# Kernel optimization log

Measured on AMD Instinct MI355X. Metric: run time of the kernel, lower is better.

Reference implementation:

```python
import jax, jax.numpy as jnp
import numpy as np

V, T, C, H, L = 32000, 1024, 768, 12, 6
HS = C // H
B = 4
EPS = 1e-5


def layernorm(x, g, b):
    mu = jnp.mean(x, axis=-1, keepdims=True)
    var = jnp.mean(jnp.square(x - mu), axis=-1, keepdims=True)
    return (x - mu) * jax.lax.rsqrt(var + EPS) * g + b


def setup_inputs() -> dict:
    key = jax.random.key(0)
    ks = iter(jax.random.split(key, 24))
    s = lambda *sh: jax.random.normal(next(ks), sh, dtype=jnp.float32) * 0.02
    inp = {
        "tokens": jax.random.randint(next(ks), (B, T), 0, V, dtype=jnp.int64),
        "tok_emb": s(V, C),
        "pos_emb": s(T, C),
        "ln1_g": jnp.ones((L, C), jnp.float32), "ln1_b": jnp.zeros((L, C), jnp.float32),
        "wq": s(L, C, C), "wk": s(L, C, C), "wv": s(L, C, C),
        "wo": s(L, C, C), "bo": jnp.zeros((L, C), jnp.float32),
        "ln2_g": jnp.ones((L, C), jnp.float32), "ln2_b": jnp.zeros((L, C), jnp.float32),
        "w1": s(L, C, 4 * C), "b1": jnp.zeros((L, 4 * C), jnp.float32),
        "w2": s(L, 4 * C, C), "b2": jnp.zeros((L, C), jnp.float32),
        "lnf_g": jnp.ones((C,), jnp.float32), "lnf_b": jnp.zeros((C,), jnp.float32),
        "lm_w": s(C, V), "lm_b": jnp.zeros((V,), jnp.float32),
    }
    return inp


def reference(tokens, tok_emb, pos_emb, ln1_g, ln1_b, wq, wk, wv, wo, bo,
              ln2_g, ln2_b, w1, b1, w2, b2, lnf_g, lnf_b, lm_w, lm_b):
    x = tok_emb[tokens] + pos_emb[:T]  # [B,T,C]
    causal = jnp.tril(jnp.ones((T, T), bool))
    scale = HS ** -0.5
    for l in range(L):
        h = layernorm(x, ln1_g[l], ln1_b[l])
        q = (h @ wq[l]).reshape(B, T, H, HS)
        k = (h @ wk[l]).reshape(B, T, H, HS)
        v = (h @ wv[l]).reshape(B, T, H, HS)
        att = jnp.einsum("bthd,bshd->bhts", q, k) * scale
        att = jnp.where(causal, att, -jnp.inf)
        wei = jax.nn.softmax(att, axis=-1)
        o = jnp.einsum("bhts,bshd->bthd", wei, v).reshape(B, T, C)
        x = o @ wo[l] + bo[l] + x
        h2 = layernorm(x, ln2_g[l], ln2_b[l])
        x = jax.nn.relu(h2 @ w1[l] + b1[l]) @ w2[l] + b2[l] + x
    x = layernorm(x, lnf_g, lnf_b)
    logits = x @ lm_w + lm_b  # [B,T,V]
    return logits
```

## Files before the change

kernel.cpp:

```cpp
#include <hip/hip_runtime.h>

static constexpr int kV = 32000, kT = 1024, kC = 768, kH = 12, kL = 6, kB = 4;
static constexpr int kF = 3072;
static constexpr int kM = kB * kT;
static constexpr float kNEG = -30000.f;

typedef __attribute__((ext_vector_type(8))) __bf16 bf16x8;
typedef __attribute__((ext_vector_type(4))) float  f32x4;

#define DEV __device__ __forceinline__

DEV void gload16(const void* g, void* l) {
  __builtin_amdgcn_global_load_lds((__attribute__((address_space(1))) void*)(g),
                                   (__attribute__((address_space(3))) void*)(l), 16, 0, 0);
}

__global__ __launch_bounds__(192) void embed_k(const int* __restrict__ tokens,
                                               const float* __restrict__ tok_emb,
                                               const float* __restrict__ pos_emb,
                                               float* __restrict__ x) {
  int row = blockIdx.x, tid = threadIdx.x;
  int tok = tokens[row];
  int t   = row & (kT - 1);
  const float4* te = (const float4*)(tok_emb + (size_t)tok * kC);
  const float4* pe = (const float4*)(pos_emb + (size_t)t * kC);
  float4 a = te[tid], p = pe[tid];
  float4 r; r.x = a.x + p.x; r.y = a.y + p.y; r.z = a.z + p.z; r.w = a.w + p.w;
  ((float4*)(x + (size_t)row * kC))[tid] = r;
}

__global__ __launch_bounds__(256) void ln_k(const float* __restrict__ x,
                                            const float* __restrict__ g,
                                            const float* __restrict__ b,
                                            __bf16* __restrict__ out) {
  int row = blockIdx.x, tid = threadIdx.x;
  const float* xr = x + (size_t)row * kC;
  float v0 = xr[tid], v1 = xr[tid + 256], v2 = xr[tid + 512];
  float s = v0 + v1 + v2;
#pragma unroll
  for (int m = 1; m < 64; m <<= 1) s += __shfl_xor(s, m, 64);
  __shared__ float red1[4], red2[4];
  int wid = tid >> 6;
  if ((tid & 63) == 0) red1[wid] = s;
  __syncthreads();
  float mu = (red1[0] + red1[1] + red1[2] + red1[3]) * (1.f / kC);
  float d0 = v0 - mu, d1 = v1 - mu, d2 = v2 - mu;
  float q = d0 * d0 + d1 * d1 + d2 * d2;
#pragma unroll
  for (int m = 1; m < 64; m <<= 1) q += __shfl_xor(q, m, 64);
  if ((tid & 63) == 0) red2[wid] = q;
  __syncthreads();
  float var = (red2[0] + red2[1] + red2[2] + red2[3]) * (1.f / kC);
  float rs = rsqrtf(var + 1e-5f);
  __bf16* o = out + (size_t)row * kC;
  o[tid]       = (__bf16)(d0 * rs * g[tid]       + b[tid]);
  o[tid + 256] = (__bf16)(d1 * rs * g[tid + 256] + b[tid + 256]);
  o[tid + 512] = (__bf16)(d2 * rs * g[tid + 512] + b[tid + 512]);
}

__global__ __launch_bounds__(256) void convT_k(const float* __restrict__ in,
                                               __bf16* __restrict__ out,
                                               int R, int Cc, size_t in_ls, size_t out_ls) {
  __shared__ float tile[32][33];
  const float* inp  = in  + (size_t)blockIdx.z * in_ls;
  __bf16*      outp = out + (size_t)blockIdx.z * out_ls;
  int r0 = blockIdx.y * 32, c0 = blockIdx.x * 32;
  int tx = threadIdx.x & 31, ty = threadIdx.x >> 5;
#pragma unroll
  for (int i = 0; i < 32; i += 8)
    tile[ty + i][tx] = inp[(size_t)(r0 + ty + i) * Cc + c0 + tx];
  __syncthreads();
#pragma unroll
  for (int i = 0; i < 32; i += 8)
    outp[(size_t)(c0 + ty + i) * R + r0 + tx] = (__bf16)tile[tx][ty + i];
}

DEV void tile_decode(int gx, int gy, int& mt, int& nt) {
  int nwg  = gx * gy;
  int wgid = blockIdx.y * gx + blockIdx.x;
  int q8 = nwg >> 3;
  int xcd = wgid & 7, loc = wgid >> 3;
  int sid = xcd * q8 + loc;
  int band = gx << 3;
  int c = sid / band, rem = sid % band;
  nt = rem >> 3;
  mt = (c << 3) + (rem & 7);
}

__global__ __launch_bounds__(512, 1) void gemmHD_k(const __bf16* __restrict__ A,
                                                   const __bf16* __restrict__ Bt,
                                                   const float* __restrict__ bias,
                                                   float* __restrict__ Cout,
                                                   int M, int N, int K) {
  __shared__ char lds[131072];
  int tid = threadIdx.x, lane = tid & 63, wid = tid >> 6;
  int wm = wid >> 2, wn = wid & 3;
  int mt, ntile;
  tile_decode(gridDim.x, gridDim.y, mt, ntile);
  int m0 = mt * 256, n0 = ntile * 256;
  int fr = lane & 15, fg = lane >> 4;
  f32x4 acc[8][4] = {};
  const size_t ldab = (size_t)K * 2;
  int nt = K >> 6;

  auto STAGE = [&](char* base, int t) {
    int k0 = t << 6;
#pragma unroll
    for (int it = 0; it < 4; ++it) {
      int oo  = tid * 16 + it * 8192;
      int row = oo >> 7;
      int cb  = (oo & 127) ^ ((row & 7) << 4);
      gload16((const char*)A + (size_t)(m0 + row) * ldab + (size_t)k0 * 2 + cb,
              base + it * 8192 + wid * 1024);
    }
#pragma unroll
    for (int it = 0; it < 4; ++it) {
      int oo  = tid * 16 + it * 8192;
      int row = oo >> 7;
      int cb  = (oo & 127) ^ ((row & 7) << 4);
      gload16((const char*)Bt + (size_t)(n0 + row) * ldab + (size_t)k0 * 2 + cb,
              base + 32768 + it * 8192 + wid * 1024);
    }
  };

  STAGE(lds, 0);
  asm volatile("s_waitcnt vmcnt(0)" ::: "memory");
  __builtin_amdgcn_sched_barrier(0);
  __builtin_amdgcn_s_barrier();

  for (int t = 0; t < nt; ++t) {
    char* base = lds + (t & 1) * 65536;
    const char* Ab = base;
    const char* Bb = base + 32768;
    if (t + 1 < nt) STAGE(lds + ((t + 1) & 1) * 65536, t + 1);

    __builtin_amdgcn_s_setprio(1);
    bf16x8 bfr[4];
#pragma unroll
    for (int p = 0; p < 4; ++p) {
      const int ks = p >> 1, mh = p & 1;
      const int cc = ks * 64 + fg * 16;
      if (mh == 0) {
#pragma unroll
        for (int n = 0; n < 4; ++n) {
          int row = wn * 64 + n * 16 + fr;
          bfr[n] = *(const bf16x8*)(Bb + row * 128 + (cc ^ ((row & 7) << 4)));
        }
      }
      bf16x8 af[4];
#pragma unroll
      for (int i = 0; i < 4; ++i) {
        int row = wm * 128 + mh * 64 + i * 16 + fr;
        af[i] = *(const bf16x8*)(Ab + row * 128 + (cc ^ ((row & 7) << 4)));
      }
#pragma unroll
      for (int i = 0; i < 4; ++i)
#pragma unroll
        for (int n = 0; n < 4; ++n)
          acc[mh * 4 + i][n] = __builtin_amdgcn_mfma_f32_16x16x32_bf16(
              af[i], bfr[n], acc[mh * 4 + i][n], 0, 0, 0);
    }
    __builtin_amdgcn_s_setprio(0);

    __builtin_amdgcn_s_barrier();
    if (t + 1 < nt)
      asm volatile("s_waitcnt vmcnt(0)" ::: "memory");
    __builtin_amdgcn_sched_barrier(0);
    __builtin_amdgcn_s_barrier();
  }

#pragma unroll
  for (int mi = 0; mi < 8; ++mi) {
#pragma unroll
    for (int n = 0; n < 4; ++n) {
      int cg  = n0 + wn * 64 + n * 16 + fr;
      int rgb = m0 + wm * 128 + mi * 16 + fg * 4;
      float bv = bias[cg];
#pragma unroll
      for (int r = 0; r < 4; ++r)
        Cout[(size_t)(rgb + r) * N + cg] = acc[mi][n][r] + bv;
    }
  }
}

template <int EPI>
__global__ __launch_bounds__(256) void gemm128_k(const __bf16* __restrict__ A,
                                                 const __bf16* __restrict__ Bt,
                                                 const float* __restrict__ bias,
                                                 const float* res,
                                                 void* Cout,
                                                 int M, int N, int K) {
  __shared__ char lds[65536];
  int tid = threadIdx.x, lane = tid & 63, wid = tid >> 6;
  int wr = wid >> 1, wc = wid & 1;
  int mt, ntile;
  tile_decode(gridDim.x, gridDim.y, mt, ntile);
  int m0 = mt * 128, n0 = ntile * 128;
  int fr = lane & 15, fg = lane >> 4;
  f32x4 acc[4][4] = {};
  const size_t ldab = (size_t)K * 2;

  auto STAGE = [&](int buf, int t) {
    int k0 = t << 6;
    char* base = lds + buf * 32768;
#pragma unroll
    for (int it = 0; it < 4; ++it) {
      int oo  = tid * 16 + it * 4096;
      int row = oo >> 7;
      int cb  = (oo & 127) ^ ((row & 7) << 4);
      gload16((const char*)A  + (size_t)(m0 + row) * ldab + (size_t)k0 * 2 + cb,
              base + it * 4096 + wid * 1024);
      gload16((const char*)Bt + (size_t)(n0 + row) * ldab + (size_t)k0 * 2 + cb,
              base + 16384 + it * 4096 + wid * 1024);
    }
  };
  auto COMPUTE = [&](int buf) {
    char* base = lds + buf * 32768;
#pragma unroll
    for (int kk = 0; kk < 2; ++kk) {
      int cb = (kk * 64 + (fg << 4)) ^ ((lane & 7) << 4);
      bf16x8 af[4], bfr[4];
#pragma unroll
      for (int i = 0; i < 4; ++i) {
        af[i]  = *(const bf16x8*)(base         + (wr * 64 + i * 16 + fr) * 128 + cb);
        bfr[i] = *(const bf16x8*)(base + 16384 + (wc * 64 + i * 16 + fr) * 128 + cb);
      }
#pragma unroll
      for (int i = 0; i < 4; ++i)
#pragma unroll
        for (int j = 0; j < 4; ++j)
          acc[i][j] = __builtin_amdgcn_mfma_f32_16x16x32_bf16(af[i], bfr[j], acc[i][j], 0, 0, 0);
    }
  };

  int nt = K >> 6;
  STAGE(0, 0);
  STAGE(1, 1);
  asm volatile("s_waitcnt vmcnt(8)" ::: "memory");
  __builtin_amdgcn_sched_barrier(0);
  __builtin_amdgcn_s_barrier();
  int cur = 0;
  for (int t = 0; t < nt; ++t) {
    __builtin_amdgcn_s_setprio(1);
    COMPUTE(cur);
    __builtin_amdgcn_s_setprio(0);
    if (t + 1 < nt) {
      __builtin_amdgcn_s_barrier();
      if (t + 2 < nt) {
        STAGE(cur, t + 2);
        asm volatile("s_waitcnt vmcnt(8)" ::: "memory");
      } else {
        asm volatile("s_waitcnt vmcnt(0)" ::: "memory");
      }
      __builtin_amdgcn_sched_barrier(0);
      __builtin_amdgcn_s_barrier();
      cur ^= 1;
    }
  }

#pragma unroll
  for (int i = 0; i < 4; ++i) {
#pragma unroll
    for (int j = 0; j < 4; ++j) {
      int cg  = n0 + wc * 64 + j * 16 + fr;
      int rgb = m0 + wr * 64 + i * 16 + fg * 4;
      if constexpr (EPI == 4) {
        if (n0 < 1536) {
#pragma unroll
          for (int r = 0; r < 4; ++r)
            ((__bf16*)Cout)[(size_t)(rgb + r) * 1536 + cg] = (__bf16)acc[i][j][r];
        } else {
          int d = cg - 1536;
          ushort4 pk;
          unsigned short* pp = (unsigned short*)&pk;
#pragma unroll
          for (int r = 0; r < 4; ++r) {
            __bf16 bv = (__bf16)acc[i][j][r];
            pp[r] = *(unsigned short*)&bv;
          }
          __bf16* vT = (__bf16*)const_cast<float*>(res);
          *(ushort4*)(vT + (size_t)d * kM + rgb) = pk;
        }
      } else if constexpr (EPI == 1) {
        float bv = bias[cg];
#pragma unroll
        for (int r = 0; r < 4; ++r) {
          float v = acc[i][j][r] + bv;
          ((__bf16*)Cout)[(size_t)(rgb + r) * N + cg] = (__bf16)fmaxf(v, 0.f);
        }
      } else {
        float bv = bias[cg];
#pragma unroll
        for (int r = 0; r < 4; ++r) {
          float v = acc[i][j][r] + bv;
          size_t idx = (size_t)(rgb + r) * N + cg;
          ((float*)Cout)[idx] = v + res[idx];
        }
      }
    }
  }
}

__global__ __launch_bounds__(256) void attn_k(const __bf16* __restrict__ qk,
                                              const __bf16* __restrict__ vT,
                                              __bf16* __restrict__ optr) {
  __shared__ char lds[40960];
  int tid = threadIdx.x, lane = tid & 63, wid = tid >> 6;
  int qt = blockIdx.x, hh = blockIdx.y, bb = blockIdx.z;
  size_t rowbase = (size_t)bb * kT;
  int qr = qt * 64 + wid * 16;
  char* Psw = lds + 32768 + wid * 2048;

  bf16x8 qf[2];
  {
    const __bf16* p = qk + (rowbase + qr + (lane & 15)) * (2 * kC) + hh * 64 + ((lane >> 4) * 8);
    qf[0] = *(const bf16x8*)p;
    qf[1] = *(const bf16x8*)(p + 32);
  }
  f32x4 oacc[4] = {};
  float mrun[4] = {kNEG, kNEG, kNEG, kNEG};
  float lrun[4] = {0.f, 0.f, 0.f, 0.f};

  bf16x8 kr[2], vr[2];
  auto LOADT = [&](int st) {
    int s0 = st * 64;
#pragma unroll
    for (int it = 0; it < 2; ++it) {
      int oo  = tid * 16 + it * 4096;
      int row = oo >> 7;
      int cb  = (oo & 127) ^ ((row & 7) << 4);
      kr[it] = *(const bf16x8*)((const char*)qk +
                 ((rowbase + s0 + row) * (2 * kC) + kC + hh * 64) * 2 + cb);
      vr[it] = *(const bf16x8*)((const char*)vT +
                 ((size_t)(hh * 64 + row) * kM + rowbase + s0) * 2 + cb);
    }
  };
  auto WRITET = [&](int buf) {
    char* b = lds + buf * 16384;
#pragma unroll
    for (int it = 0; it < 2; ++it) {
      int oo = tid * 16 + it * 4096;
      *(bf16x8*)(b + oo)        = kr[it];
      *(bf16x8*)(b + 8192 + oo) = vr[it];
    }
  };

  LOADT(0);
  WRITET(0);
  if (qt >= 1) LOADT(1);

  for (int st = 0; st <= qt; ++st) {
    int cur = st & 1;
    char* kb = lds + cur * 16384;
    char* vb = kb + 8192;
    __syncthreads();
    if (st + 1 <= qt) {
      WRITET(cur ^ 1);
      if (st + 2 <= qt) LOADT(st + 2);
    }

    int s0 = st * 64;
    f32x4 sacc[4] = {};
#pragma unroll
    for (int kk = 0; kk < 2; ++kk) {
      int cb = (kk * 64 + ((lane >> 4) << 4)) ^ ((lane & 7) << 4);
#pragma unroll
      for (int j = 0; j < 4; ++j) {
        bf16x8 kf = *(const bf16x8*)(kb + (j * 16 + (lane & 15)) * 128 + cb);
        sacc[j] = __builtin_amdgcn_mfma_f32_16x16x32_bf16(qf[kk], kf, sacc[j], 0, 0, 0);
      }
    }

    float pv[4][4], vm[4] = {kNEG, kNEG, kNEG, kNEG};
#pragma unroll
    for (int j = 0; j < 4; ++j) {
      int scol = s0 + j * 16 + (lane & 15);
#pragma unroll
      for (int r = 0; r < 4; ++r) {
        int qrow = qr + (lane >> 4) * 4 + r;
        float sv = sacc[j][r] * 0.125f;
        if (scol > qrow) sv = kNEG;
        pv[j][r] = sv;
        vm[r] = fmaxf(vm[r], sv);
      }
    }
#pragma unroll
    for (int r = 0; r < 4; ++r) {
      float v = vm[r];
      v = fmaxf(v, __shfl_xor(v, 1, 64)); v = fmaxf(v, __shfl_xor(v, 2, 64));
      v = fmaxf(v, __shfl_xor(v, 4, 64)); v = fmaxf(v, __shfl_xor(v, 8, 64));
      float mnew = fmaxf(mrun[r], v);
      float sc = __expf(mrun[r] - mnew);
      mrun[r] = mnew;
      lrun[r] *= sc;
      oacc[0][r] *= sc; oacc[1][r] *= sc; oacc[2][r] *= sc; oacc[3][r] *= sc;
      float rsum = 0.f;
#pragma unroll
      for (int j = 0; j < 4; ++j) {
        float p = __expf(pv[j][r] - mnew);
        pv[j][r] = p;
        rsum += p;
      }
      rsum += __shfl_xor(rsum, 1, 64); rsum += __shfl_xor(rsum, 2, 64);
      rsum += __shfl_xor(rsum, 4, 64); rsum += __shfl_xor(rsum, 8, 64);
      lrun[r] += rsum;
    }

#pragma unroll
    for (int j = 0; j < 4; ++j)
#pragma unroll
      for (int r = 0; r < 4; ++r) {
        int rloc = (lane >> 4) * 4 + r;
        int cbyt = (2 * (j * 16 + (lane & 15))) ^ ((rloc & 7) << 4);
        *(__bf16*)(Psw + rloc * 128 + cbyt) = (__bf16)pv[j][r];
      }

#pragma unroll
    for (int kk = 0; kk < 2; ++kk) {
      int cb = (kk * 64 + ((lane >> 4) << 4)) ^ ((lane & 7) << 4);
      bf16x8 pf = *(const bf16x8*)(Psw + (lane & 15) * 128 + cb);
#pragma unroll
      for (int j = 0; j < 4; ++j) {
        bf16x8 vf = *(const bf16x8*)(vb + (j * 16 + (lane & 15)) * 128 + cb);
        oacc[j] = __builtin_amdgcn_mfma_f32_16x16x32_bf16(pf, vf, oacc[j], 0, 0, 0);
      }
    }
  }

#pragma unroll
  for (int r = 0; r < 4; ++r) {
    float inv = lrun[r] > 0.f ? 1.f / lrun[r] : 0.f;
#pragma unroll
    for (int j = 0; j < 4; ++j) {
      int cg = hh * 64 + j * 16 + (lane & 15);
      int rg = qr + (lane >> 4) * 4 + r;
      optr[(rowbase + rg) * kC + cg] = (__bf16)(oacc[j][r] * inv);
    }
  }
}

extern "C" void kernel_launch(void* const* d_in, const int* in_sizes, int n_in,
                              void* d_out, int out_size, void* d_ws, size_t ws_size,
                              hipStream_t stream) {
  (void)in_sizes; (void)n_in; (void)out_size; (void)ws_size;
  const int*   tokens  = (const int*)  d_in[0];
  const float* tok_emb = (const float*)d_in[1];
  const float* pos_emb = (const float*)d_in[2];
  const float* ln1_g   = (const float*)d_in[3];
  const float* ln1_b   = (const float*)d_in[4];
  const float* wq      = (const float*)d_in[5];
  const float* wk      = (const float*)d_in[6];
  const float* wv      = (const float*)d_in[7];
  const float* wo      = (const float*)d_in[8];
  const float* bo      = (const float*)d_in[9];
  const float* ln2_g   = (const float*)d_in[10];
  const float* ln2_b   = (const float*)d_in[11];
  const float* w1      = (const float*)d_in[12];
  const float* b1      = (const float*)d_in[13];
  const float* w2      = (const float*)d_in[14];
  const float* b2      = (const float*)d_in[15];
  const float* lnf_g   = (const float*)d_in[16];
  const float* lnf_b   = (const float*)d_in[17];
  const float* lm_w    = (const float*)d_in[18];
  const float* lm_b    = (const float*)d_in[19];
  float* out = (float*)d_out;

  char* ws = (char*)d_ws;
  size_t off = 0;
  auto alloc = [&](size_t bytes) -> char* {
    char* p = ws + off; off += (bytes + 255) & ~(size_t)255; return p;
  };
  float*  x    = (float*) alloc((size_t)kM * kC * 4);
  __bf16* h    = (__bf16*)alloc((size_t)kM * kC * 2);
  __bf16* qkvT = (__bf16*)alloc((size_t)kL * 3 * kC * kC * 2);
  __bf16* woT  = (__bf16*)alloc((size_t)kL * kC * kC * 2);
  __bf16* w1T  = (__bf16*)alloc((size_t)kL * kC * kF * 2);
  __bf16* w2T  = (__bf16*)alloc((size_t)kL * kC * kF * 2);
  __bf16* qkb  = (__bf16*)alloc((size_t)kM * 2 * kC * 2);
  __bf16* vTb  = (__bf16*)alloc((size_t)kC * kM * 2);
  __bf16* ob   = (__bf16*)alloc((size_t)kM * kC * 2);
  __bf16* ffb  = (__bf16*)alloc((size_t)kM * kF * 2);
  __bf16* lmwT = qkb;

  dim3 blk(256), blk512(512);
  convT_k<<<dim3(kC/32, kC/32, kL), blk, 0, stream>>>(wq, qkvT,           kC, kC, (size_t)kC*kC, (size_t)3*kC*kC);
  convT_k<<<dim3(kC/32, kC/32, kL), blk, 0, stream>>>(wk, qkvT + kC*kC,   kC, kC, (size_t)kC*kC, (size_t)3*kC*kC);
  convT_k<<<dim3(kC/32, kC/32, kL), blk, 0, stream>>>(wv, qkvT + 2*kC*kC, kC, kC, (size_t)kC*kC, (size_t)3*kC*kC);
  convT_k<<<dim3(kC/32, kC/32, kL), blk, 0, stream>>>(wo, woT,            kC, kC, (size_t)kC*kC, (size_t)kC*kC);
  convT_k<<<dim3(kF/32, kC/32, kL), blk, 0, stream>>>(w1, w1T,            kC, kF, (size_t)kC*kF, (size_t)kC*kF);
  convT_k<<<dim3(kC/32, kF/32, kL), blk, 0, stream>>>(w2, w2T,            kF, kC, (size_t)kC*kF, (size_t)kC*kF);

  embed_k<<<kM, 192, 0, stream>>>(tokens, tok_emb, pos_emb, x);

  for (int l = 0; l < kL; ++l) {
    ln_k<<<kM, 256, 0, stream>>>(x, ln1_g + l*kC, ln1_b + l*kC, h);
    gemm128_k<4><<<dim3(3*kC/128, kM/128), blk, 0, stream>>>(
        h, qkvT + (size_t)l*3*kC*kC, nullptr, (const float*)vTb, qkb, kM, 3*kC, kC);
    attn_k<<<dim3(kT/64, kH, kB), blk, 0, stream>>>(qkb, vTb, ob);
    gemm128_k<2><<<dim3(kC/128, kM/128), blk, 0, stream>>>(ob, woT + (size_t)l*kC*kC, bo + l*kC, x, x, kM, kC, kC);
    ln_k<<<kM, 256, 0, stream>>>(x, ln2_g + l*kC, ln2_b + l*kC, h);
    gemm128_k<1><<<dim3(kF/128, kM/128), blk, 0, stream>>>(h, w1T + (size_t)l*kC*kF, b1 + l*kF, nullptr, ffb, kM, kF, kC);
    gemm128_k<2><<<dim3(kC/128, kM/128), blk, 0, stream>>>(ffb, w2T + (size_t)l*kC*kF, b2 + l*kC, x, x, kM, kC, kF);
  }
  convT_k<<<dim3(kV/32, kC/32, 1), blk, 0, stream>>>(lm_w, lmwT, kC, kV, 0, 0);
  ln_k<<<kM, 256, 0, stream>>>(x, lnf_g, lnf_b, h);
  gemmHD_k<<<dim3(kV/256, kM/256), blk512, 0, stream>>>(h, lmwT, lm_b, out, kM, kV, kC);
}
```

Before: 1.476 ms.

## Switch LM-head GEMM to a four-stage BK=32 LDS pipeline

The 256x256 GEMM kernel (gemmHD_k) is restructured from two LDS buffers with a K-step of 64 into four 32 KB buffers with a K-step of 32. Three stages are kept in flight, and partial vmcnt waits replace full drains. The goal is to hide more global-load latency behind MFMA work. In exchange, it drops the XOR swizzle on LDS rows, which risks bank conflicts on the fragment reads, and it doubles the number of barrier round-trips over K.

```diff
diff --git a/kernel.cpp b/kernel.cpp
--- a/kernel.cpp
+++ b/kernel.cpp
@@ -101,72 +101,61 @@
   int fr = lane & 15, fg = lane >> 4;
   f32x4 acc[8][4] = {};
   const size_t ldab = (size_t)K * 2;
-  int nt = K >> 6;
-
-  auto STAGE = [&](char* base, int t) {
-    int k0 = t << 6;
-#pragma unroll
-    for (int it = 0; it < 4; ++it) {
+  int nt = K >> 5;
+
+  auto STAGE = [&](int buf, int t) {
+    int k0 = t << 5;
+    char* base = lds + buf * 32768;
+#pragma unroll
+    for (int it = 0; it < 2; ++it) {
       int oo  = tid * 16 + it * 8192;
-      int row = oo >> 7;
-      int cb  = (oo & 127) ^ ((row & 7) << 4);
-      gload16((const char*)A + (size_t)(m0 + row) * ldab + (size_t)k0 * 2 + cb,
+      int row = oo >> 6;
+      int cb  = oo & 63;
+      gload16((const char*)A  + (size_t)(m0 + row) * ldab + (size_t)k0 * 2 + cb,
               base + it * 8192 + wid * 1024);
-    }
-#pragma unroll
-    for (int it = 0; it < 4; ++it) {
-      int oo  = tid * 16 + it * 8192;
-      int row = oo >> 7;
-      int cb  = (oo & 127) ^ ((row & 7) << 4);
       gload16((const char*)Bt + (size_t)(n0 + row) * ldab + (size_t)k0 * 2 + cb,
-              base + 32768 + it * 8192 + wid * 1024);
-    }
-  };
-
-  STAGE(lds, 0);
-  asm volatile("s_waitcnt vmcnt(0)" ::: "memory");
+              base + 16384 + it * 8192 + wid * 1024);
+    }
+  };
+
+  auto COMPUTE = [&](int buf) {
+    const char* Ab = lds + buf * 32768;
+    const char* Bb = Ab + 16384;
+    bf16x8 bfr[4];
+#pragma unroll
+    for (int n = 0; n < 4; ++n)
+      bfr[n] = *(const bf16x8*)(Bb + (wn * 64 + n * 16 + fr) * 64 + fg * 16);
+#pragma unroll
+    for (int mi = 0; mi < 8; ++mi) {
+      bf16x8 af = *(const bf16x8*)(Ab + (wm * 128 + mi * 16 + fr) * 64 + fg * 16);
+#pragma unroll
+      for (int n = 0; n < 4; ++n)
+        acc[mi][n] = __builtin_amdgcn_mfma_f32_16x16x32_bf16(af, bfr[n], acc[mi][n], 0, 0, 0);
+    }
+  };
+
+  STAGE(0, 0);
+  if (nt > 1) STAGE(1, 1);
+  if (nt > 2) STAGE(2, 2);
+  if (nt > 2)      asm volatile("s_waitcnt vmcnt(8)" ::: "memory");
+  else if (nt > 1) asm volatile("s_waitcnt vmcnt(4)" ::: "memory");
+  else             asm volatile("s_waitcnt vmcnt(0)" ::: "memory");
   __builtin_amdgcn_sched_barrier(0);
   __builtin_amdgcn_s_barrier();
 
   for (int t = 0; t < nt; ++t) {
-    char* base = lds + (t & 1) * 65536;
-    const char* Ab = base;
-    const char* Bb = base + 32768;
-    if (t + 1 < nt) STAGE(lds + ((t + 1) & 1) * 65536, t + 1);
-
+    if (t + 3 < nt) STAGE((t + 3) & 3, t + 3);
     __builtin_amdgcn_s_setprio(1);
-    bf16x8 bfr[4];
-#pragma unroll
-    for (int p = 0; p < 4; ++p) {
-      const int ks = p >> 1, mh = p & 1;
-      const int cc = ks * 64 + fg * 16;
-      if (mh == 0) {
-#pragma unroll
-        for (int n = 0; n < 4; ++n) {
-          int row = wn * 64 + n * 16 + fr;
-          bfr[n] = *(const bf16x8*)(Bb + row * 128 + (cc ^ ((row & 7) << 4)));
-        }
-      }
-      bf16x8 af[4];
-#pragma unroll
-      for (int i = 0; i < 4; ++i) {
-        int row = wm * 128 + mh * 64 + i * 16 + fr;
-        af[i] = *(const bf16x8*)(Ab + row * 128 + (cc ^ ((row & 7) << 4)));
-      }
-#pragma unroll
-      for (int i = 0; i < 4; ++i)
-#pragma unroll
-        for (int n = 0; n < 4; ++n)
-          acc[mh * 4 + i][n] = __builtin_amdgcn_mfma_f32_16x16x32_bf16(
-              af[i], bfr[n], acc[mh * 4 + i][n], 0, 0, 0);
-    }
+    COMPUTE(t & 3);
     __builtin_amdgcn_s_setprio(0);
-
-    __builtin_amdgcn_s_barrier();
-    if (t + 1 < nt)
-      asm volatile("s_waitcnt vmcnt(0)" ::: "memory");
-    __builtin_amdgcn_sched_barrier(0);
-    __builtin_amdgcn_s_barrier();
+    if (t + 1 < nt) {
+      __builtin_amdgcn_s_barrier();
+      if (t + 3 < nt)      asm volatile("s_waitcnt vmcnt(8)" ::: "memory");
+      else if (t + 2 < nt) asm volatile("s_waitcnt vmcnt(4)" ::: "memory");
+      else                 asm volatile("s_waitcnt vmcnt(0)" ::: "memory");
+      __builtin_amdgcn_sched_barrier(0);
+      __builtin_amdgcn_s_barrier();
+    }
   }
 
 #pragma unroll
```

Result: no change. 1.496 ms (+1.3%).
